# Kernel optimization log

Measured on AMD Instinct MI355X. Metric: run time of the kernel, lower is better.

Reference implementation:

```python
import jax, jax.numpy as jnp
import numpy as np

D_MODEL = 1024
N_HEADS = 16
HEAD_DIM = D_MODEL // N_HEADS
WINDOW = 128
ROPE_BASE = 10000.0


def _rope_cos_sin(T, dim, dtype):
    inv_freq = 1.0 / (ROPE_BASE ** (jnp.arange(0, dim, 2, dtype=jnp.float32) / dim))
    freqs = jnp.arange(T, dtype=jnp.float32)[:, None] * inv_freq[None, :]  # [T, dim/2]
    emb = jnp.concatenate([freqs, freqs], axis=-1)  # [T, dim]
    return jnp.cos(emb).astype(dtype), jnp.sin(emb).astype(dtype)


def _rotate_half(x):
    h = x.shape[-1] // 2
    return jnp.concatenate([-x[..., h:], x[..., :h]], axis=-1)


def _apply_rotary(x, cos, sin):
    # x: [B, T, H, Dh]; cos/sin: [T, Dh]
    c = cos[None, :, None, :]
    s = sin[None, :, None, :]
    return x * c + _rotate_half(x) * s


def setup_inputs() -> dict:
    key = jax.random.key(0)
    ks = jax.random.split(key, 6)
    B, T = 2, 2048
    query = jax.random.normal(ks[0], (B, T, D_MODEL), dtype=jnp.float32)
    scale = 1.0 / np.sqrt(D_MODEL)
    Wq = jax.random.normal(ks[1], (D_MODEL, D_MODEL), dtype=jnp.float32) * scale
    Wk = jax.random.normal(ks[2], (D_MODEL, D_MODEL), dtype=jnp.float32) * scale
    Wv = jax.random.normal(ks[3], (D_MODEL, D_MODEL), dtype=jnp.float32) * scale
    Wo = jax.random.normal(ks[4], (D_MODEL, D_MODEL), dtype=jnp.float32) * scale
    bo = jax.random.normal(ks[5], (D_MODEL,), dtype=jnp.float32) * 0.01
    return {"query": query, "Wq": Wq, "Wk": Wk, "Wv": Wv, "Wo": Wo, "bo": bo}


def reference(query, Wq, Wk, Wv, Wo, bo):
    # Sliding-window causal self-attention with rotary embeddings (eval mode, no dropout).
    B, T, D = query.shape
    H, Dh = N_HEADS, HEAD_DIM
    sm_scale = Dh ** -0.5

    # Projections (torch nn.Linear: y = x @ W.T)
    q = (query @ Wq.T).reshape(B, T, H, Dh)
    k = (query @ Wk.T).reshape(B, T, H, Dh)
    v = (query @ Wv.T).reshape(B, T, H, Dh)

    cos, sin = _rope_cos_sin(T, Dh, query.dtype)
    q = _apply_rotary(q, cos, sin)
    k = _apply_rotary(k, cos, sin)

    # [B, H, T, Dh]
    q = q.transpose(0, 2, 1, 3)
    k = k.transpose(0, 2, 1, 3)
    v = v.transpose(0, 2, 1, 3)

    scores = jnp.einsum('bhqd,bhkd->bhqk', q, k) * sm_scale

    # Causal sliding-window mask: masked if j > i or j < i - (WINDOW - 1)
    i = jnp.arange(T)[:, None]
    j = jnp.arange(T)[None, :]
    mask = (j > i) | (j < i - (WINDOW - 1))  # [T, T], True = masked
    scores = jnp.where(mask[None, None], jnp.float32(-jnp.inf), scores)

    attn = jax.nn.softmax(scores, axis=-1)
    out = jnp.einsum('bhqk,bhkd->bhqd', attn, v)  # [B, H, T, Dh]
    out = out.transpose(0, 2, 1, 3).reshape(B, T, D)
    return out @ Wo.T + bo
```

## Files before the change

### kernel.cpp

```cpp
#include <hip/hip_runtime.h>

#define BATCH 2
#define SEQ   2048
#define DMODEL 1024
#define NHEADS 16
#define HDIM   64
#define WINDOW 128
#define ROWS  (BATCH * SEQ)

typedef __bf16 bf16x8 __attribute__((ext_vector_type(8)));
typedef __bf16 bf16x4 __attribute__((ext_vector_type(4)));
typedef float  f32x4  __attribute__((ext_vector_type(4)));

__device__ __forceinline__ void async_load16(const __bf16* g, __bf16* l) {
    __builtin_amdgcn_global_load_lds(
        (const __attribute__((address_space(1))) unsigned int*)g,
        (__attribute__((address_space(3))) unsigned int*)l, 16, 0, 0);
}

__global__ __launch_bounds__(256) void convert_bf16(
    const float* __restrict__ X,
    const float* __restrict__ Wq, const float* __restrict__ Wk,
    const float* __restrict__ Wv, const float* __restrict__ Wo,
    __bf16* __restrict__ Xbf, __bf16* __restrict__ Wbf,
    float* __restrict__ ct, float* __restrict__ st)
{
    const int XN = ROWS * DMODEL / 4;
    const int WN = DMODEL * DMODEL / 4;
    const int TOT = XN + 4 * WN;
    int idx = blockIdx.x * blockDim.x + threadIdx.x;

    if (idx < TOT) {
        const float* src;
        __bf16* dst;
        if (idx < XN) {
            src = X + (size_t)idx * 4;
            dst = Xbf + (size_t)idx * 4;
        } else {
            int rel = idx - XN;
            int w = rel / WN;
            int off = rel - w * WN;
            const float* Wp = (w == 0) ? Wq : (w == 1) ? Wk : (w == 2) ? Wv : Wo;
            src = Wp + (size_t)off * 4;
            dst = Wbf + (size_t)rel * 4;
        }
        float4 v = *(const float4*)src;
        bf16x4 o;
        o[0] = (__bf16)v.x; o[1] = (__bf16)v.y; o[2] = (__bf16)v.z; o[3] = (__bf16)v.w;
        *(bf16x4*)dst = o;
    } else if (idx < TOT + SEQ * 32) {
        int k = idx - TOT;
        int t = k >> 5, d = k & 31;
        float ang = (float)t * expf(-(float)d * 0.28782313662425572f);
        float s, c;
        sincosf(ang, &s, &c);
        ct[k] = c; st[k] = s;
    }
}

template<int TM>
__device__ __forceinline__ void gemm_mfma_body(
    const __bf16* __restrict__ A, const __bf16* __restrict__ B,
    void* __restrict__ Cout, const float* __restrict__ bias,
    const float* __restrict__ ct, const float* __restrict__ st,
    int mode, int N, int K, int m0, int n0)
{
    constexpr int NI = TM / 32;
    __shared__ __bf16 As[2][TM * 32];
    __shared__ __bf16 Bs[2][128 * 32];

    const int tid  = threadIdx.x;
    const int lane = tid & 63;
    const int wv   = tid >> 6;
    const int wrow = (wv >> 1) * (TM / 2);
    const int wcol = (wv & 1) * 64;

    const int srow = lane >> 2;
    const int schk = (lane & 3) ^ ((lane >> 3) & 3);
    const int arbase = (TM == 128) ? 32 * wv : 16 * wv;
    const int brbase = 32 * wv;

    const __bf16* gA0 = A + (size_t)(m0 + arbase + srow) * K + 8 * schk;
    const __bf16* gA1 = gA0 + (size_t)16 * K;
    const __bf16* gB0 = B + (size_t)(n0 + brbase + srow) * K + 8 * schk;
    const __bf16* gB1 = gB0 + (size_t)16 * K;

    const int frow = lane & 15;
    const int fsw  = 8 * ((lane >> 4) ^ ((frow >> 1) & 3));

    f32x4 acc[NI][4];
#pragma unroll
    for (int i = 0; i < NI; ++i)
#pragma unroll
        for (int j = 0; j < 4; ++j) {
            acc[i][j][0] = 0.f; acc[i][j][1] = 0.f;
            acc[i][j][2] = 0.f; acc[i][j][3] = 0.f;
        }

    for (int k0 = 0; k0 < K; k0 += 64) {
        __syncthreads();
#pragma unroll
        for (int h = 0; h < 2; ++h) {
            async_load16(gA0 + k0 + 32 * h, As[h] + arbase * 32);
            if (TM == 128)
                async_load16(gA1 + k0 + 32 * h, As[h] + (arbase + 16) * 32);
            async_load16(gB0 + k0 + 32 * h, Bs[h] + brbase * 32);
            async_load16(gB1 + k0 + 32 * h, Bs[h] + (brbase + 16) * 32);
        }
        __syncthreads();

#pragma unroll
        for (int h = 0; h < 2; ++h) {
            bf16x8 afr[NI], bfr[4];
#pragma unroll
            for (int i = 0; i < NI; ++i)
                afr[i] = *(const bf16x8*)(As[h] + (wrow + 16 * i + frow) * 32 + fsw);
#pragma unroll
            for (int j = 0; j < 4; ++j)
                bfr[j] = *(const bf16x8*)(Bs[h] + (wcol + 16 * j + frow) * 32 + fsw);
#pragma unroll
            for (int i = 0; i < NI; ++i)
#pragma unroll
                for (int j = 0; j < 4; ++j)
                    acc[i][j] = __builtin_amdgcn_mfma_f32_16x16x32_bf16(
                        afr[i], bfr[j], acc[i][j], 0, 0, 0);
        }
    }

#pragma unroll
    for (int i = 0; i < NI; ++i) {
#pragma unroll
        for (int r = 0; r < 4; ++r) {
            int row = m0 + wrow + i * 16 + (lane >> 4) * 4 + r;
            if (mode <= 1) {
                int t = row & (SEQ - 1);
#pragma unroll
                for (int j = 0; j < 2; ++j) {
                    int dd = j * 16 + (lane & 15);
                    float c = ct[t * 32 + dd];
                    float s = st[t * 32 + dd];
                    float v0 = acc[i][j][r], v1 = acc[i][j + 2][r];
                    float n0v = v0 * c - v1 * s;
                    float n1v = v1 * c + v0 * s;
                    if (mode == 0) { n0v *= 0.125f; n1v *= 0.125f; }
                    acc[i][j][r] = n0v; acc[i][j + 2][r] = n1v;
                }
            }
#pragma unroll
            for (int j = 0; j < 4; ++j) {
                int col = n0 + wcol + j * 16 + (lane & 15);
                float v = acc[i][j][r];
                if (mode == 3)
                    ((float*)Cout)[(size_t)row * N + col] = v + bias[col];
                else
                    ((__bf16*)Cout)[(size_t)row * N + col] = (__bf16)v;
            }
        }
    }
}

__global__ __launch_bounds__(256) void gemm_qkv_bf(
    const __bf16* __restrict__ X, const __bf16* __restrict__ Wbf,
    __bf16* __restrict__ Qb, __bf16* __restrict__ Kb, __bf16* __restrict__ Vb,
    const float* __restrict__ ct, const float* __restrict__ st)
{
    const int z = blockIdx.z;
    const __bf16* W = Wbf + (size_t)z * (DMODEL * DMODEL);
    __bf16* C = (z == 0) ? Qb : (z == 1) ? Kb : Vb;
    gemm_mfma_body<128>(X, W, C, nullptr, ct, st, z, DMODEL, DMODEL,
                        blockIdx.y * 128, blockIdx.x * 128);
}

__global__ __launch_bounds__(256) void gemm_out_bf(
    const __bf16* __restrict__ Abf, const __bf16* __restrict__ Wo,
    const float* __restrict__ bias, float* __restrict__ out)
{
    gemm_mfma_body<64>(Abf, Wo, out, bias, nullptr, nullptr, 3, DMODEL, DMODEL,
                       blockIdx.y * 64, blockIdx.x * 128);
}

#define QTILE 64
#define KPAD  72
#define VPAD  216
#define PPAD  168

__global__ __launch_bounds__(256) void attn_mfma(
    const __bf16* __restrict__ Qb, const __bf16* __restrict__ Kb,
    const __bf16* __restrict__ Vb, __bf16* __restrict__ Abf)
{
    __shared__ __bf16 KsPs[192 * KPAD];
    __shared__ __bf16 Vt[64 * VPAD];

    const int tid  = threadIdx.x;
    const int lane = tid & 63;
    const int wv   = tid >> 6;
    const int q0   = blockIdx.x * QTILE;
    const int h    = blockIdx.y;
    const int b    = blockIdx.z;
    const int jbase = q0 - 128;
    const size_t hoff = (size_t)h * HDIM;
    const int nloc  = lane & 15;
    const int mbase = (lane >> 4) * 4;
    const int fk    = (lane >> 4) * 8;

    const __bf16* Kg = Kb + (size_t)(b * SEQ) * DMODEL + hoff;
    const __bf16* Vg = Vb + (size_t)(b * SEQ) * DMODEL + hoff;

#pragma unroll
    for (int it = 0; it < 6; ++it) {
        int idx = tid + it * 256;
        int jt = idx >> 3;
        int dq = (idx & 7) * 8;
        int jg = jbase + jt;
        int jc = jg < 0 ? 0 : jg;
        bf16x8 kv = *(const bf16x8*)(Kg + (size_t)jc * DMODEL + dq);
        bf16x8 vv = *(const bf16x8*)(Vg + (size_t)jc * DMODEL + dq);
        *(bf16x8*)(KsPs + jt * KPAD + dq) = kv;
#pragma unroll
        for (int e = 0; e < 8; ++e) Vt[(dq + e) * VPAD + jt] = vv[e];
    }
#pragma unroll
    for (int it = 0; it < 4; ++it) {
        int idx = tid + it * 256;
        int d = idx >> 4, c = idx & 15;
        Vt[d * VPAD + 192 + c] = (__bf16)0.0f;
    }
    __syncthreads();

    const __bf16* Qg = Qb + (size_t)(b * SEQ + q0 + 16 * wv + nloc) * DMODEL + hoff + fk;
    bf16x8 qfr0 = *(const bf16x8*)(Qg);
    bf16x8 qfr1 = *(const bf16x8*)(Qg + 32);

    f32x4 s[9];
#pragma unroll
    for (int c = 0; c < 9; ++c) {
        const __bf16* kp = KsPs + (size_t)(16 * (wv + c) + nloc) * KPAD + fk;
        bf16x8 k0 = *(const bf16x8*)kp;
        bf16x8 k1 = *(const bf16x8*)(kp + 32);
        f32x4 z; z[0] = 0.f; z[1] = 0.f; z[2] = 0.f; z[3] = 0.f;
        z = __builtin_amdgcn_mfma_f32_16x16x32_bf16(qfr0, k0, z, 0, 0, 0);
        z = __builtin_amdgcn_mfma_f32_16x16x32_bf16(qfr1, k1, z, 0, 0, 0);
        s[c] = z;
    }
    __syncthreads();

    float inv_row[4];
#pragma unroll
    for (int r = 0; r < 4; ++r) {
        int rl = 16 * wv + mbase + r;
        float mx = -INFINITY;
#pragma unroll
        for (int c = 0; c < 9; ++c) {
            int jt = 16 * (wv + c) + nloc;
            bool valid = (jt >= rl + 1) && (jt <= rl + 128) && (jbase + jt >= 0);
            float sv = valid ? s[c][r] : -INFINITY;
            s[c][r] = sv;
            mx = fmaxf(mx, sv);
        }
#pragma unroll
        for (int off = 8; off; off >>= 1) mx = fmaxf(mx, __shfl_xor(mx, off));
        float sum = 0.f;
#pragma unroll
        for (int c = 0; c < 9; ++c) {
            float p = __expf(s[c][r] - mx);
            s[c][r] = p;
            sum += p;
        }
#pragma unroll
        for (int off = 8; off; off >>= 1) sum += __shfl_xor(sum, off);
        inv_row[r] = 1.0f / sum;
    }

    __bf16* myP = KsPs + (size_t)wv * 16 * PPAD;
#pragma unroll
    for (int c = 0; c < 9; ++c)
#pragma unroll
        for (int r = 0; r < 4; ++r)
            myP[(mbase + r) * PPAD + 16 * c + nloc] = (__bf16)(s[c][r] * inv_row[r]);
#pragma unroll
    for (int r = 0; r < 4; ++r)
        myP[(mbase + r) * PPAD + 144 + nloc] = (__bf16)0.0f;

    asm volatile("" ::: "memory");
    __builtin_amdgcn_s_waitcnt(0);

    f32x4 o[4];
#pragma unroll
    for (int j = 0; j < 4; ++j) { o[j][0] = 0.f; o[j][1] = 0.f; o[j][2] = 0.f; o[j][3] = 0.f; }
#pragma unroll
    for (int stp = 0; stp < 5; ++stp) {
        bf16x8 pf = *(const bf16x8*)(myP + nloc * PPAD + 32 * stp + fk);
#pragma unroll
        for (int j = 0; j < 4; ++j) {
            bf16x8 vf = *(const bf16x8*)(Vt + (size_t)(16 * j + nloc) * VPAD
                                         + 16 * wv + 32 * stp + fk);
            o[j] = __builtin_amdgcn_mfma_f32_16x16x32_bf16(pf, vf, o[j], 0, 0, 0);
        }
    }

    __bf16* Og = Abf + (size_t)(b * SEQ + q0 + 16 * wv) * DMODEL + hoff;
#pragma unroll
    for (int j = 0; j < 4; ++j)
#pragma unroll
        for (int r = 0; r < 4; ++r)
            Og[(size_t)(mbase + r) * DMODEL + 16 * j + nloc] = (__bf16)o[j][r];
}

extern "C" void kernel_launch(void* const* d_in, const int* in_sizes, int n_in,
                              void* d_out, int out_size, void* d_ws, size_t ws_size,
                              hipStream_t stream)
{
    const float* X  = (const float*)d_in[0];
    const float* Wq = (const float*)d_in[1];
    const float* Wk = (const float*)d_in[2];
    const float* Wv = (const float*)d_in[3];
    const float* Wo = (const float*)d_in[4];
    const float* bo = (const float*)d_in[5];
    float* out = (float*)d_out;

    const size_t MB = 1ull << 20;
    __bf16* Xbf = (__bf16*)d_ws;
    __bf16* Wbf = (__bf16*)((char*)d_ws + 8 * MB);
    __bf16* Qb  = (__bf16*)((char*)d_ws + 16 * MB);
    __bf16* Kb  = (__bf16*)((char*)d_ws + 24 * MB);
    __bf16* Vb  = (__bf16*)((char*)d_ws + 32 * MB);
    float*  ctab = (float*)((char*)d_ws + 40 * MB);
    float*  stab = (float*)((char*)d_ws + 41 * MB);
    __bf16* Abf = Xbf;

    {
        int total = (ROWS * DMODEL + 4 * DMODEL * DMODEL) / 4 + SEQ * 32;
        convert_bf16<<<(total + 255) / 256, 256, 0, stream>>>(
            X, Wq, Wk, Wv, Wo, Xbf, Wbf, ctab, stab);
    }
    {
        dim3 grid(DMODEL / 128, ROWS / 128, 3);
        gemm_qkv_bf<<<grid, 256, 0, stream>>>(Xbf, Wbf, Qb, Kb, Vb, ctab, stab);
    }
    {
        dim3 grid(SEQ / QTILE, NHEADS, BATCH);
        attn_mfma<<<grid, 256, 0, stream>>>(Qb, Kb, Vb, Abf);
    }
    {
        dim3 grid(DMODEL / 128, ROWS / 64, 1);
        gemm_out_bf<<<grid, 256, 0, stream>>>(Abf, Wbf + 3ull * DMODEL * DMODEL, bo, out);
    }
}
```

Baseline: 169.0 us.

## Fuse all stages into one persistent kernel with software grid barriers

Replaces the four separate launches (convert, QKV GEMM, attention, output GEMM) with a single persistent kernel of 512 blocks that runs each stage in turn, separated by atomic-counter grid barriers. GEMM tiles become 128x64 with a 128-wide K step, and each block handles fixed QKV/output tiles and two attention units. This removes launch gaps and tail effects between stages. In exchange it adds barrier spin and fence cost, relies on all 512 blocks being co-resident (two per CU), and uses smaller GEMM tiles with less reuse.

```diff
diff --git a/kernel.cpp b/kernel.cpp
--- a/kernel.cpp
+++ b/kernel.cpp
@@ -7,6 +7,7 @@
 #define HDIM   64
 #define WINDOW 128
 #define ROWS  (BATCH * SEQ)
+#define NBLK  512
 
 typedef __bf16 bf16x8 __attribute__((ext_vector_type(8)));
 typedef __bf16 bf16x4 __attribute__((ext_vector_type(4)));
@@ -18,108 +19,79 @@
         (__attribute__((address_space(3))) unsigned int*)l, 16, 0, 0);
 }
 
-__global__ __launch_bounds__(256) void convert_bf16(
-    const float* __restrict__ X,
-    const float* __restrict__ Wq, const float* __restrict__ Wk,
-    const float* __restrict__ Wv, const float* __restrict__ Wo,
-    __bf16* __restrict__ Xbf, __bf16* __restrict__ Wbf,
-    float* __restrict__ ct, float* __restrict__ st)
-{
-    const int XN = ROWS * DMODEL / 4;
-    const int WN = DMODEL * DMODEL / 4;
-    const int TOT = XN + 4 * WN;
-    int idx = blockIdx.x * blockDim.x + threadIdx.x;
-
-    if (idx < TOT) {
-        const float* src;
-        __bf16* dst;
-        if (idx < XN) {
-            src = X + (size_t)idx * 4;
-            dst = Xbf + (size_t)idx * 4;
+__device__ __forceinline__ void grid_barrier(unsigned* cnt, unsigned* gen)
+{
+    __syncthreads();
+    __threadfence_system();
+    if (threadIdx.x == 0) {
+        unsigned g = atomicAdd(gen, 0u);
+        if (atomicAdd(cnt, 1u) == NBLK - 1) {
+            atomicExch(cnt, 0u);
+            atomicAdd(gen, 1u);
         } else {
-            int rel = idx - XN;
-            int w = rel / WN;
-            int off = rel - w * WN;
-            const float* Wp = (w == 0) ? Wq : (w == 1) ? Wk : (w == 2) ? Wv : Wo;
-            src = Wp + (size_t)off * 4;
-            dst = Wbf + (size_t)rel * 4;
-        }
-        float4 v = *(const float4*)src;
-        bf16x4 o;
-        o[0] = (__bf16)v.x; o[1] = (__bf16)v.y; o[2] = (__bf16)v.z; o[3] = (__bf16)v.w;
-        *(bf16x4*)dst = o;
-    } else if (idx < TOT + SEQ * 32) {
-        int k = idx - TOT;
-        int t = k >> 5, d = k & 31;
-        float ang = (float)t * expf(-(float)d * 0.28782313662425572f);
-        float s, c;
-        sincosf(ang, &s, &c);
-        ct[k] = c; st[k] = s;
-    }
-}
-
-template<int TM>
-__device__ __forceinline__ void gemm_mfma_body(
+            while (atomicAdd(gen, 0u) == g) __builtin_amdgcn_s_sleep(2);
+        }
+    }
+    __syncthreads();
+    __threadfence_system();
+}
+
+__device__ __forceinline__ void gemm_tile(
+    __bf16* Asb, __bf16* Bsb,
     const __bf16* __restrict__ A, const __bf16* __restrict__ B,
     void* __restrict__ Cout, const float* __restrict__ bias,
     const float* __restrict__ ct, const float* __restrict__ st,
     int mode, int N, int K, int m0, int n0)
 {
-    constexpr int NI = TM / 32;
-    __shared__ __bf16 As[2][TM * 32];
-    __shared__ __bf16 Bs[2][128 * 32];
-
     const int tid  = threadIdx.x;
     const int lane = tid & 63;
     const int wv   = tid >> 6;
-    const int wrow = (wv >> 1) * (TM / 2);
-    const int wcol = (wv & 1) * 64;
+    const int wrow = wv * 32;
 
     const int srow = lane >> 2;
     const int schk = (lane & 3) ^ ((lane >> 3) & 3);
-    const int arbase = (TM == 128) ? 32 * wv : 16 * wv;
-    const int brbase = 32 * wv;
+    const int arbase = wv * 32;
+    const int brbase = wv * 16;
 
     const __bf16* gA0 = A + (size_t)(m0 + arbase + srow) * K + 8 * schk;
     const __bf16* gA1 = gA0 + (size_t)16 * K;
     const __bf16* gB0 = B + (size_t)(n0 + brbase + srow) * K + 8 * schk;
-    const __bf16* gB1 = gB0 + (size_t)16 * K;
 
     const int frow = lane & 15;
     const int fsw  = 8 * ((lane >> 4) ^ ((frow >> 1) & 3));
 
-    f32x4 acc[NI][4];
-#pragma unroll
-    for (int i = 0; i < NI; ++i)
+    f32x4 acc[2][4];
+#pragma unroll
+    for (int i = 0; i < 2; ++i)
 #pragma unroll
         for (int j = 0; j < 4; ++j) {
             acc[i][j][0] = 0.f; acc[i][j][1] = 0.f;
             acc[i][j][2] = 0.f; acc[i][j][3] = 0.f;
         }
 
-    for (int k0 = 0; k0 < K; k0 += 64) {
+    for (int k0 = 0; k0 < K; k0 += 128) {
         __syncthreads();
 #pragma unroll
-        for (int h = 0; h < 2; ++h) {
-            async_load16(gA0 + k0 + 32 * h, As[h] + arbase * 32);
-            if (TM == 128)
-                async_load16(gA1 + k0 + 32 * h, As[h] + (arbase + 16) * 32);
-            async_load16(gB0 + k0 + 32 * h, Bs[h] + brbase * 32);
-            async_load16(gB1 + k0 + 32 * h, Bs[h] + (brbase + 16) * 32);
+        for (int h = 0; h < 4; ++h) {
+            async_load16(gA0 + k0 + 32 * h, Asb + h * (128 * 32) + arbase * 32);
+            async_load16(gA1 + k0 + 32 * h, Asb + h * (128 * 32) + (arbase + 16) * 32);
+            async_load16(gB0 + k0 + 32 * h, Bsb + h * (64 * 32) + brbase * 32);
         }
         __syncthreads();
 
 #pragma unroll
-        for (int h = 0; h < 2; ++h) {
-            bf16x8 afr[NI], bfr[4];
-#pragma unroll
-            for (int i = 0; i < NI; ++i)
-                afr[i] = *(const bf16x8*)(As[h] + (wrow + 16 * i + frow) * 32 + fsw);
+        for (int h = 0; h < 4; ++h) {
+            const __bf16* Ah = Asb + h * (128 * 32);
+            const __bf16* Bh = Bsb + h * (64 * 32);
+            bf16x8 afr[2], bfr[4];
+#pragma unroll
+            for (int i = 0; i < 2; ++i)
+                afr[i] = *(const bf16x8*)(Ah + (wrow + 16 * i + frow) * 32 + fsw);
 #pragma unroll
             for (int j = 0; j < 4; ++j)
-                bfr[j] = *(const bf16x8*)(Bs[h] + (wcol + 16 * j + frow) * 32 + fsw);
-#pragma unroll
-            for (int i = 0; i < NI; ++i)
+                bfr[j] = *(const bf16x8*)(Bh + (16 * j + frow) * 32 + fsw);
+#pragma unroll
+            for (int i = 0; i < 2; ++i)
 #pragma unroll
                 for (int j = 0; j < 4; ++j)
                     acc[i][j] = __builtin_amdgcn_mfma_f32_16x16x32_bf16(
@@ -128,7 +100,7 @@
     }
 
 #pragma unroll
-    for (int i = 0; i < NI; ++i) {
+    for (int i = 0; i < 2; ++i) {
 #pragma unroll
         for (int r = 0; r < 4; ++r) {
             int row = m0 + wrow + i * 16 + (lane >> 4) * 4 + r;
@@ -148,7 +120,7 @@
             }
 #pragma unroll
             for (int j = 0; j < 4; ++j) {
-                int col = n0 + wcol + j * 16 + (lane & 15);
+                int col = n0 + j * 16 + (lane & 15);
                 float v = acc[i][j][r];
                 if (mode == 3)
                     ((float*)Cout)[(size_t)row * N + col] = v + bias[col];
@@ -159,52 +131,35 @@
     }
 }
 
-__global__ __launch_bounds__(256) void gemm_qkv_bf(
-    const __bf16* __restrict__ X, const __bf16* __restrict__ Wbf,
-    __bf16* __restrict__ Qb, __bf16* __restrict__ Kb, __bf16* __restrict__ Vb,
-    const float* __restrict__ ct, const float* __restrict__ st)
-{
-    const int z = blockIdx.z;
-    const __bf16* W = Wbf + (size_t)z * (DMODEL * DMODEL);
-    __bf16* C = (z == 0) ? Qb : (z == 1) ? Kb : Vb;
-    gemm_mfma_body<128>(X, W, C, nullptr, ct, st, z, DMODEL, DMODEL,
-                        blockIdx.y * 128, blockIdx.x * 128);
-}
-
-__global__ __launch_bounds__(256) void gemm_out_bf(
-    const __bf16* __restrict__ Abf, const __bf16* __restrict__ Wo,
-    const float* __restrict__ bias, float* __restrict__ out)
-{
-    gemm_mfma_body<64>(Abf, Wo, out, bias, nullptr, nullptr, 3, DMODEL, DMODEL,
-                       blockIdx.y * 64, blockIdx.x * 128);
-}
-
 #define QTILE 64
 #define KPAD  72
 #define VPAD  216
 #define PPAD  168
 
-__global__ __launch_bounds__(256) void attn_mfma(
+__device__ __forceinline__ void attn_unit(
+    char* sm, int u,
     const __bf16* __restrict__ Qb, const __bf16* __restrict__ Kb,
     const __bf16* __restrict__ Vb, __bf16* __restrict__ Abf)
 {
-    __shared__ __bf16 KsPs[192 * KPAD];
-    __shared__ __bf16 Vt[64 * VPAD];
+    __bf16* KsPs = (__bf16*)sm;
+    __bf16* Vt   = KsPs + 192 * KPAD;
 
     const int tid  = threadIdx.x;
     const int lane = tid & 63;
     const int wv   = tid >> 6;
-    const int q0   = blockIdx.x * QTILE;
-    const int h    = blockIdx.y;
-    const int b    = blockIdx.z;
+    const int q0   = (u & 31) * QTILE;
+    const int h    = (u >> 5) & 15;
+    const int bb   = u >> 9;
     const int jbase = q0 - 128;
     const size_t hoff = (size_t)h * HDIM;
     const int nloc  = lane & 15;
     const int mbase = (lane >> 4) * 4;
     const int fk    = (lane >> 4) * 8;
 
-    const __bf16* Kg = Kb + (size_t)(b * SEQ) * DMODEL + hoff;
-    const __bf16* Vg = Vb + (size_t)(b * SEQ) * DMODEL + hoff;
+    const __bf16* Kg = Kb + (size_t)(bb * SEQ) * DMODEL + hoff;
+    const __bf16* Vg = Vb + (size_t)(bb * SEQ) * DMODEL + hoff;
+
+    __syncthreads();
 
 #pragma unroll
     for (int it = 0; it < 6; ++it) {
@@ -227,7 +182,7 @@
     }
     __syncthreads();
 
-    const __bf16* Qg = Qb + (size_t)(b * SEQ + q0 + 16 * wv + nloc) * DMODEL + hoff + fk;
+    const __bf16* Qg = Qb + (size_t)(bb * SEQ + q0 + 16 * wv + nloc) * DMODEL + hoff + fk;
     bf16x8 qfr0 = *(const bf16x8*)(Qg);
     bf16x8 qfr1 = *(const bf16x8*)(Qg + 32);
 
@@ -298,12 +253,93 @@
         }
     }
 
-    __bf16* Og = Abf + (size_t)(b * SEQ + q0 + 16 * wv) * DMODEL + hoff;
+    __bf16* Og = Abf + (size_t)(bb * SEQ + q0 + 16 * wv) * DMODEL + hoff;
 #pragma unroll
     for (int j = 0; j < 4; ++j)
 #pragma unroll
         for (int r = 0; r < 4; ++r)
             Og[(size_t)(mbase + r) * DMODEL + 16 * j + nloc] = (__bf16)o[j][r];
+}
+
+__global__ __launch_bounds__(256, 2) void fused_all(
+    const float* __restrict__ X,
+    const float* __restrict__ Wq, const float* __restrict__ Wk,
+    const float* __restrict__ Wv, const float* __restrict__ Wo,
+    const float* __restrict__ bo, float* __restrict__ out,
+    __bf16* __restrict__ Xbf, __bf16* __restrict__ Wbf,
+    __bf16* __restrict__ Qb, __bf16* __restrict__ Kb, __bf16* __restrict__ Vb,
+    __bf16* __restrict__ Abf, float* __restrict__ ct, float* __restrict__ st,
+    unsigned* bar)
+{
+    __shared__ __align__(16) char smem[55296];
+    __bf16* As = (__bf16*)smem;
+    __bf16* Bs = As + 4 * 128 * 32;
+    unsigned* cnt = bar;
+    unsigned* gen = bar + 1;
+
+    const int b   = blockIdx.x;
+    const int tid = threadIdx.x;
+
+    {
+        const int XN = ROWS * DMODEL / 4;
+        const int WN = DMODEL * DMODEL / 4;
+        const int TOT = XN + 4 * WN;
+        const int LIM = TOT + SEQ * 32;
+        for (int base = 0; base < LIM; base += NBLK * 256) {
+            int idx = base + b * 256 + tid;
+            if (idx < TOT) {
+                const float* src;
+                __bf16* dst;
+                if (idx < XN) {
+                    src = X + (size_t)idx * 4;
+                    dst = Xbf + (size_t)idx * 4;
+                } else {
+                    int rel = idx - XN;
+                    int w = rel / WN;
+                    int off = rel - w * WN;
+                    const float* Wp = (w == 0) ? Wq : (w == 1) ? Wk
+                                    : (w == 2) ? Wv : Wo;
+                    src = Wp + (size_t)off * 4;
+                    dst = Wbf + (size_t)rel * 4;
+                }
+                float4 v = *(const float4*)src;
+                bf16x4 o;
+                o[0] = (__bf16)v.x; o[1] = (__bf16)v.y;
+                o[2] = (__bf16)v.z; o[3] = (__bf16)v.w;
+                *(bf16x4*)dst = o;
+            } else if (idx < LIM) {
+                int k = idx - TOT;
+                int t = k >> 5, d = k & 31;
+                float ang = (float)t * expf(-(float)d * 0.28782313662425572f);
+                float s, c;
+                sincosf(ang, &s, &c);
+                ct[k] = c; st[k] = s;
+            }
+        }
+    }
+    grid_barrier(cnt, gen);
+
+    {
+        const int x = (b >> 3) & 15;
+        const int y = 4 * (b & 7) + (b >> 7);
+        for (int z = 0; z < 3; ++z) {
+            __bf16* C = (z == 0) ? Qb : (z == 1) ? Kb : Vb;
+            gemm_tile(As, Bs, Xbf, Wbf + (size_t)z * DMODEL * DMODEL,
+                      C, nullptr, ct, st, z, DMODEL, DMODEL, y * 128, x * 64);
+        }
+    }
+    grid_barrier(cnt, gen);
+
+    attn_unit(smem, b,        Qb, Kb, Vb, Abf);
+    attn_unit(smem, b + NBLK, Qb, Kb, Vb, Abf);
+    grid_barrier(cnt, gen);
+
+    {
+        const int x = (b >> 3) & 15;
+        const int y = 4 * (b & 7) + (b >> 7);
+        gemm_tile(As, Bs, Abf, Wbf + 3ull * DMODEL * DMODEL,
+                  out, bo, nullptr, nullptr, 3, DMODEL, DMODEL, y * 128, x * 64);
+    }
 }
 
 extern "C" void kernel_launch(void* const* d_in, const int* in_sizes, int n_in,
@@ -326,23 +362,12 @@
     __bf16* Vb  = (__bf16*)((char*)d_ws + 32 * MB);
     float*  ctab = (float*)((char*)d_ws + 40 * MB);
     float*  stab = (float*)((char*)d_ws + 41 * MB);
-    __bf16* Abf = Xbf;
-
-    {
-        int total = (ROWS * DMODEL + 4 * DMODEL * DMODEL) / 4 + SEQ * 32;
-        convert_bf16<<<(total + 255) / 256, 256, 0, stream>>>(
-            X, Wq, Wk, Wv, Wo, Xbf, Wbf, ctab, stab);
-    }
-    {
-        dim3 grid(DMODEL / 128, ROWS / 128, 3);
-        gemm_qkv_bf<<<grid, 256, 0, stream>>>(Xbf, Wbf, Qb, Kb, Vb, ctab, stab);
-    }
-    {
-        dim3 grid(SEQ / QTILE, NHEADS, BATCH);
-        attn_mfma<<<grid, 256, 0, stream>>>(Qb, Kb, Vb, Abf);
-    }
-    {
-        dim3 grid(DMODEL / 128, ROWS / 64, 1);
-        gemm_out_bf<<<grid, 256, 0, stream>>>(Abf, Wbf + 3ull * DMODEL * DMODEL, bo, out);
-    }
-}
+    __bf16* Abf = (__bf16*)((char*)d_ws + 42 * MB);
+    unsigned* bar = (unsigned*)((char*)d_ws + 50 * MB);
+
+    hipMemsetAsync(bar, 0, 64, stream);
+
+    fused_all<<<NBLK, 256, 0, stream>>>(
+        X, Wq, Wk, Wv, Wo, bo, out,
+        Xbf, Wbf, Qb, Kb, Vb, Abf, ctab, stab, bar);
+}
```

After: 501.1 us. 196% more time.
